# Kernel optimization log

Measured on AMD Instinct MI355X. Metric: run time of the kernel, lower is better.

Reference implementation:

```python
import jax, jax.numpy as jnp
import numpy as np

NUM_NUM = 32    # numerical (pass-through) features
NUM_CAT = 32    # embedded categorical features
CARD = 128      # one-hot width per categorical feature
OUT = 32        # per-feature embedding output dim (0.25 * 128)
BATCH = 16384


def setup_inputs() -> dict:
    key = jax.random.key(0)
    k1, k2, k3 = jax.random.split(key, 3)
    x = jax.random.normal(k1, (BATCH, NUM_NUM + NUM_CAT * CARD), dtype=jnp.float32)
    # stacked per-feature nn.Linear(CARD, OUT) weights/biases (all same shape)
    W = jax.random.normal(k2, (NUM_CAT, CARD, OUT), dtype=jnp.float32) / np.sqrt(CARD).astype(np.float32)
    b = jax.random.normal(k3, (NUM_CAT, OUT), dtype=jnp.float32) * 0.01
    return {"x": x, "W": W, "b": b}


def reference(x, W, b):
    # Numerical columns pass through unchanged; each categorical one-hot slice
    # goes through its own small Linear, then everything is concatenated.
    # Since all categorical slices have identical width, the per-feature loop of
    # small GEMMs is expressed as one batched (block-diagonal) matmul.
    x_num = x[..., :NUM_NUM]                                      # [B, 32]
    x_cat = x[..., NUM_NUM:].reshape(x.shape[:-1] + (NUM_CAT, CARD))  # [B, F, C]
    emb = jnp.einsum('bfc,fco->bfo', x_cat, W) + b                # [B, F, OUT]
    emb = emb.reshape(x.shape[:-1] + (NUM_CAT * OUT,))            # [B, 1024]
    return jnp.concatenate([x_num, emb], axis=-1)                 # [B, 1056]
```

## Files before the change

kernel.cpp:

```cpp
#include <hip/hip_runtime.h>

#define BATCH   16384
#define NUM_NUM 32
#define NUM_CAT 32
#define CARD    128
#define OUT_F   32
#define XSTRIDE (NUM_NUM + NUM_CAT * CARD)
#define OSTRIDE (NUM_NUM + NUM_CAT * OUT_F)

#define TR   256
#define CK   32
#define XPAD (CK + 1)

__global__ __launch_bounds__(256, 1) void emb_gemm(const float* __restrict__ x,
                                                   const float* __restrict__ W,
                                                   const float* __restrict__ bias,
                                                   float* __restrict__ out) {
    __shared__ float w_s[CARD][OUT_F];
    __shared__ float x_s[TR][XPAD];

    const int f    = blockIdx.y;
    const int row0 = blockIdx.x * TR;
    const int tid  = threadIdx.x;

    {
        const float4* wg  = (const float4*)(W + (size_t)f * CARD * OUT_F);
        float4*       ws4 = (float4*)&w_s[0][0];
#pragma unroll
        for (int i = 0; i < 4; ++i) ws4[i * 256 + tid] = wg[i * 256 + tid];
    }

    const int og = tid & 7;
    const int rg = tid >> 3;

    float acc[8][4];
#pragma unroll
    for (int j = 0; j < 8; ++j)
#pragma unroll
        for (int k = 0; k < 4; ++k) acc[j][k] = 0.0f;

    const float* xg_base = x + (size_t)row0 * XSTRIDE + NUM_NUM + f * CARD;

    for (int ck = 0; ck < CARD / CK; ++ck) {
        const float* xg = xg_base + ck * CK;
#pragma unroll
        for (int it = 0; it < 8; ++it) {
            int    idx = it * 256 + tid;
            int    r   = idx >> 3;
            int    c4  = (idx & 7) * 4;
            float4 v   = *(const float4*)(xg + (size_t)r * XSTRIDE + c4);
            x_s[r][c4 + 0] = v.x;
            x_s[r][c4 + 1] = v.y;
            x_s[r][c4 + 2] = v.z;
            x_s[r][c4 + 3] = v.w;
        }
        __syncthreads();

#pragma unroll 8
        for (int c = 0; c < CK; ++c) {
            float4 w4 = *(const float4*)&w_s[ck * CK + c][og * 4];
#pragma unroll
            for (int j = 0; j < 8; ++j) {
                float xv = x_s[rg * 8 + j][c];
                acc[j][0] += xv * w4.x;
                acc[j][1] += xv * w4.y;
                acc[j][2] += xv * w4.z;
                acc[j][3] += xv * w4.w;
            }
        }
        __syncthreads();
    }

    float4 b4 = *(const float4*)(bias + f * OUT_F + og * 4);
#pragma unroll
    for (int j = 0; j < 8; ++j) {
        int    row = row0 + rg * 8 + j;
        float4 o4;
        o4.x = acc[j][0] + b4.x;
        o4.y = acc[j][1] + b4.y;
        o4.z = acc[j][2] + b4.z;
        o4.w = acc[j][3] + b4.w;
        *(float4*)(out + (size_t)row * OSTRIDE + NUM_NUM + f * OUT_F + og * 4) = o4;
    }
}

__global__ __launch_bounds__(256) void num_copy(const float* __restrict__ x,
                                                float* __restrict__ out) {
    int    idx = blockIdx.x * 256 + threadIdx.x;
    int    row = idx >> 3;
    int    c4  = (idx & 7) * 4;
    float4 v   = *(const float4*)(x + (size_t)row * XSTRIDE + c4);
    *(float4*)(out + (size_t)row * OSTRIDE + c4) = v;
}

extern "C" void kernel_launch(void* const* d_in, const int* in_sizes, int n_in,
                              void* d_out, int out_size, void* d_ws, size_t ws_size,
                              hipStream_t stream) {
    const float* x    = (const float*)d_in[0];
    const float* W    = (const float*)d_in[1];
    const float* bias = (const float*)d_in[2];
    float*       out  = (float*)d_out;

    dim3 grid(BATCH / TR, NUM_CAT);
    emb_gemm<<<grid, 256, 0, stream>>>(x, W, bias, out);
    num_copy<<<BATCH * 8 / 256, 256, 0, stream>>>(x, out);
}
```

Measured before the change: 95.89 us.

## Replace tiled shared-memory GEMM with per-row register GEMV and fused copy

Each thread now computes all 32 outputs of one row for one feature, reading x directly as float4 and W via uniform global loads instead of staging both in shared memory. The numeric pass-through copy is folded into the blocks handling the first feature, removing the second launch. This removes shared-memory traffic and barriers. In exchange, x loads become strided across threads (one row per lane), which hurts coalescing.

Result: slower. 169.3 us (+76.5%).

```diff
diff --git a/kernel.cpp b/kernel.cpp
--- a/kernel.cpp
+++ b/kernel.cpp
@@ -5,92 +5,59 @@
 #define NUM_CAT 32
 #define CARD    128
 #define OUT_F   32
-#define XSTRIDE (NUM_NUM + NUM_CAT * CARD)
-#define OSTRIDE (NUM_NUM + NUM_CAT * OUT_F)
+#define XSTRIDE 4128
+#define OSTRIDE 1056
 
-#define TR   256
-#define CK   32
-#define XPAD (CK + 1)
-
-__global__ __launch_bounds__(256, 1) void emb_gemm(const float* __restrict__ x,
-                                                   const float* __restrict__ W,
+__global__ __launch_bounds__(256, 4) void emb_gemv(const float* __restrict__ x,
+                                                   const float* __restrict__ Wm,
                                                    const float* __restrict__ bias,
                                                    float* __restrict__ out) {
-    __shared__ float w_s[CARD][OUT_F];
-    __shared__ float x_s[TR][XPAD];
+    const int f   = blockIdx.y;
+    const int row = blockIdx.x * 256 + threadIdx.x;
 
-    const int f    = blockIdx.y;
-    const int row0 = blockIdx.x * TR;
-    const int tid  = threadIdx.x;
+    const float4* __restrict__ wq = (const float4*)(Wm + (size_t)f * (CARD * OUT_F));
+    const float*  __restrict__ xr = x + (size_t)row * XSTRIDE + NUM_NUM + f * CARD;
 
-    {
-        const float4* wg  = (const float4*)(W + (size_t)f * CARD * OUT_F);
-        float4*       ws4 = (float4*)&w_s[0][0];
+    float acc[32];
 #pragma unroll
-        for (int i = 0; i < 4; ++i) ws4[i * 256 + tid] = wg[i * 256 + tid];
+    for (int k = 0; k < 32; ++k) acc[k] = 0.0f;
+
+#pragma unroll 2
+    for (int c4 = 0; c4 < CARD / 4; ++c4) {
+        const float4 xv = *(const float4*)(xr + c4 * 4);
+#pragma unroll
+        for (int cc = 0; cc < 4; ++cc) {
+            const float xf = (&xv.x)[cc];
+#pragma unroll
+            for (int q = 0; q < 8; ++q) {
+                const float4 w = wq[(c4 * 4 + cc) * 8 + q];
+                acc[q * 4 + 0] += xf * w.x;
+                acc[q * 4 + 1] += xf * w.y;
+                acc[q * 4 + 2] += xf * w.z;
+                acc[q * 4 + 3] += xf * w.w;
+            }
+        }
     }
 
-    const int og = tid & 7;
-    const int rg = tid >> 3;
-
-    float acc[8][4];
+    const float4* __restrict__ bq = (const float4*)(bias + f * OUT_F);
+    float* orow = out + (size_t)row * OSTRIDE + NUM_NUM + f * OUT_F;
 #pragma unroll
-    for (int j = 0; j < 8; ++j)
-#pragma unroll
-        for (int k = 0; k < 4; ++k) acc[j][k] = 0.0f;
-
-    const float* xg_base = x + (size_t)row0 * XSTRIDE + NUM_NUM + f * CARD;
-
-    for (int ck = 0; ck < CARD / CK; ++ck) {
-        const float* xg = xg_base + ck * CK;
-#pragma unroll
-        for (int it = 0; it < 8; ++it) {
-            int    idx = it * 256 + tid;
-            int    r   = idx >> 3;
-            int    c4  = (idx & 7) * 4;
-            float4 v   = *(const float4*)(xg + (size_t)r * XSTRIDE + c4);
-            x_s[r][c4 + 0] = v.x;
-            x_s[r][c4 + 1] = v.y;
-            x_s[r][c4 + 2] = v.z;
-            x_s[r][c4 + 3] = v.w;
-        }
-        __syncthreads();
-
-#pragma unroll 8
-        for (int c = 0; c < CK; ++c) {
-            float4 w4 = *(const float4*)&w_s[ck * CK + c][og * 4];
-#pragma unroll
-            for (int j = 0; j < 8; ++j) {
-                float xv = x_s[rg * 8 + j][c];
-                acc[j][0] += xv * w4.x;
-                acc[j][1] += xv * w4.y;
-                acc[j][2] += xv * w4.z;
-                acc[j][3] += xv * w4.w;
-            }
-        }
-        __syncthreads();
+    for (int q = 0; q < 8; ++q) {
+        const float4 b = bq[q];
+        float4       o;
+        o.x = acc[q * 4 + 0] + b.x;
+        o.y = acc[q * 4 + 1] + b.y;
+        o.z = acc[q * 4 + 2] + b.z;
+        o.w = acc[q * 4 + 3] + b.w;
+        *(float4*)(orow + q * 4) = o;
     }
 
-    float4 b4 = *(const float4*)(bias + f * OUT_F + og * 4);
+    if (f == 0) {
+        const float4* src = (const float4*)(x + (size_t)row * XSTRIDE);
+        float4*       dst = (float4*)(out + (size_t)row * OSTRIDE);
 #pragma unroll
-    for (int j = 0; j < 8; ++j) {
-        int    row = row0 + rg * 8 + j;
-        float4 o4;
-        o4.x = acc[j][0] + b4.x;
-        o4.y = acc[j][1] + b4.y;
-        o4.z = acc[j][2] + b4.z;
-        o4.w = acc[j][3] + b4.w;
-        *(float4*)(out + (size_t)row * OSTRIDE + NUM_NUM + f * OUT_F + og * 4) = o4;
+        for (int q = 0; q < 8; ++q) dst[q] = src[q];
     }
-}
-
-__global__ __launch_bounds__(256) void num_copy(const float* __restrict__ x,
-                                                float* __restrict__ out) {
-    int    idx = blockIdx.x * 256 + threadIdx.x;
-    int    row = idx >> 3;
-    int    c4  = (idx & 7) * 4;
-    float4 v   = *(const float4*)(x + (size_t)row * XSTRIDE + c4);
-    *(float4*)(out + (size_t)row * OSTRIDE + c4) = v;
 }
 
 extern "C" void kernel_launch(void* const* d_in, const int* in_sizes, int n_in,
@@ -101,7 +68,6 @@
     const float* bias = (const float*)d_in[2];
     float*       out  = (float*)d_out;
 
-    dim3 grid(BATCH / TR, NUM_CAT);
-    emb_gemm<<<grid, 256, 0, stream>>>(x, W, bias, out);
-    num_copy<<<BATCH * 8 / 256, 256, 0, stream>>>(x, out);
+    dim3 grid(BATCH / 256, NUM_CAT);
+    emb_gemv<<<grid, 256, 0, stream>>>(x, W, bias, out);
 }
```
